# Kernel tuning notes

Hardware: AMD Instinct MI355X
Metric: run time of the kernel (lower is better)

The kernel has to match this reference:

```python
import jax, jax.numpy as jnp
import numpy as np

TOK_DIM = 512
POS_DIM = 512
N_HEADS = 16
HEAD_DIM = 64
D_MODEL = 1024
INNER = N_HEADS * HEAD_DIM
B, T = 4, 2048


def setup_inputs() -> dict:
    key = jax.random.key(0)
    ks = jax.random.split(key, 5)
    s = 0.02
    return {
        "x": jax.random.normal(ks[0], (B, T, TOK_DIM + POS_DIM), dtype=jnp.float32),
        "Wq": jax.random.normal(ks[1], (POS_DIM, INNER), dtype=jnp.float32) * s,
        "Wk": jax.random.normal(ks[2], (POS_DIM, INNER), dtype=jnp.float32) * s,
        "Wv": jax.random.normal(ks[3], (TOK_DIM, INNER), dtype=jnp.float32) * s,
        "Wo": jax.random.normal(ks[4], (INNER, D_MODEL), dtype=jnp.float32) * s,
    }


def reference(x, Wq, Wk, Wv, Wo):
    b, t, _ = x.shape
    x_tok = x[:, :, :TOK_DIM]
    x_pos = x[:, :, TOK_DIM:]
    # project and split heads: [B, H, T, Dh]
    q = (x_pos @ Wq).reshape(b, t, N_HEADS, HEAD_DIM).transpose(0, 2, 1, 3)
    k = (x_pos @ Wk).reshape(b, t, N_HEADS, HEAD_DIM).transpose(0, 2, 1, 3)
    v = (x_tok @ Wv).reshape(b, t, N_HEADS, HEAD_DIM).transpose(0, 2, 1, 3)
    att = jnp.einsum("bhqd,bhkd->bhqk", q, k) / jnp.sqrt(jnp.float32(HEAD_DIM))
    causal = jnp.tril(jnp.ones((t, t), dtype=bool))
    att = jnp.where(causal, att, -jnp.inf)
    att = jax.nn.softmax(att, axis=-1)
    out = jnp.einsum("bhqk,bhkd->bhqd", att, v)
    out = out.transpose(0, 2, 1, 3).reshape(b, t, INNER)
    return out @ Wo
```

## Files before the change

### kernel.cpp

```cpp
#include <hip/hip_runtime.h>
#include <stdint.h>


typedef unsigned short u16;
typedef __bf16 bf16;
typedef bf16 bf16x8 __attribute__((ext_vector_type(8)));
typedef u16 u16x8 __attribute__((ext_vector_type(8)));
typedef u16 u16x4 __attribute__((ext_vector_type(4)));
typedef float f32x4 __attribute__((ext_vector_type(4)));
typedef uint32_t u32x4 __attribute__((ext_vector_type(4)));

__device__ __forceinline__ u16 cvt_bf16(float f) {
  uint32_t u = __builtin_bit_cast(uint32_t, f);
  u += 0x7FFFu + ((u >> 16) & 1u);
  return (u16)(u >> 16);
}

__device__ __forceinline__ uint32_t pack2_bf16(float lo, float hi) {
  uint32_t a = __builtin_bit_cast(uint32_t, lo) + 0x8000u;
  uint32_t b = __builtin_bit_cast(uint32_t, hi) + 0x8000u;
  return __builtin_amdgcn_perm(b, a, 0x07060302u);
}

__device__ __forceinline__ f32x4 mfma_bf(bf16x8 a, bf16x8 b, f32x4 c) {
  return __builtin_amdgcn_mfma_f32_16x16x32_bf16(a, b, c, 0, 0, 0);
}

typedef __attribute__((address_space(1))) const uint32_t g_u32;
typedef __attribute__((address_space(3))) uint32_t l_u32;
__device__ __forceinline__ void gload16(const u16* g, u16* l) {
  __builtin_amdgcn_global_load_lds((g_u32*)g, (l_u32*)l, 16, 0, 0);
}

__global__ __launch_bounds__(256) void prep_x(
    const float* __restrict__ x, u16* __restrict__ xtok,
    u16* __restrict__ xpos) {
  int idx = blockIdx.x * 256 + threadIdx.x;
  int row = idx >> 8;
  int c4 = (idx & 255) * 4;
  float4 v = *(const float4*)(x + (size_t)row * 1024 + c4);
  u16x4 b = {cvt_bf16(v.x), cvt_bf16(v.y), cvt_bf16(v.z), cvt_bf16(v.w)};
  u16* dst = (c4 < 512) ? (xtok + (size_t)row * 512 + c4)
                        : (xpos + (size_t)row * 512 + c4 - 512);
  *(u16x4*)dst = b;
}

__global__ __launch_bounds__(256) void prep_w(
    const float* __restrict__ Wq, const float* __restrict__ Wk,
    const float* __restrict__ Wv, const float* __restrict__ Wo,
    u16* __restrict__ Wt, u16* __restrict__ WoT) {
  const int z = blockIdx.z;
  const float* src = (z == 0) ? Wq : (z == 1) ? Wk : (z == 2) ? Wv : Wo;
  const int K = (z == 3) ? 1024 : 512;
  u16* dst = (z == 3) ? WoT : (Wt + (size_t)z * 1024 * 512);
  const int k0 = blockIdx.y * 64, n0 = blockIdx.x * 64;
  if (k0 >= K) return;
  __shared__ u16 T[64][68];
  const int tid = threadIdx.x;
  const int r = tid >> 4, c = (tid & 15) * 4;
#pragma unroll
  for (int i = 0; i < 4; i++) {
    float4 v = *(const float4*)(src + (size_t)(k0 + r + i * 16) * 1024 + n0 + c);
    u16x4 b = {cvt_bf16(v.x), cvt_bf16(v.y), cvt_bf16(v.z), cvt_bf16(v.w)};
    *(u16x4*)&T[r + i * 16][c] = b;
  }
  __syncthreads();
#pragma unroll
  for (int i = 0; i < 4; i++) {
    int n = r + i * 16;
    u16x4 v;
#pragma unroll
    for (int j = 0; j < 4; j++) v[j] = T[c + j][n];
    *(u16x4*)(dst + (size_t)(n0 + n) * K + k0 + c) = v;
  }
}


#define LDA(P, S) { const u16* bp_ = rA + (P)*16384 + (S)*8192;              \
  af[0][0] = *(const bf16x8*)(bp_ + 0*1024 + colx0);                         \
  af[0][1] = *(const bf16x8*)(bp_ + 0*1024 + colx1);                         \
  af[1][0] = *(const bf16x8*)(bp_ + 1*1024 + colx0);                         \
  af[1][1] = *(const bf16x8*)(bp_ + 1*1024 + colx1);                         \
  af[2][0] = *(const bf16x8*)(bp_ + 2*1024 + colx0);                         \
  af[2][1] = *(const bf16x8*)(bp_ + 2*1024 + colx1);                         \
  af[3][0] = *(const bf16x8*)(bp_ + 3*1024 + colx0);                         \
  af[3][1] = *(const bf16x8*)(bp_ + 3*1024 + colx1); }

#define LDB(P, S, NB) { const u16* bp_ = rB + (P)*16384 + (S)*8192;          \
  bf[(NB)+0][0] = *(const bf16x8*)(bp_ + 0*1024 + colx0);                    \
  bf[(NB)+0][1] = *(const bf16x8*)(bp_ + 0*1024 + colx1);                    \
  bf[(NB)+1][0] = *(const bf16x8*)(bp_ + 1*1024 + colx0);                    \
  bf[(NB)+1][1] = *(const bf16x8*)(bp_ + 1*1024 + colx1); }

#define MM1(M_, N_, J_) { f32x4 c_ = acc[M_][N_];                            \
  c_ = mfma_bf(af[J_][0], bf[N_][0], c_);                                    \
  c_ = mfma_bf(af[J_][1], bf[N_][1], c_);                                    \
  acc[M_][N_] = c_; }

#define MM(MB, NB) MM1((MB)+0,(NB)+0,0) MM1((MB)+0,(NB)+1,0)                 \
                   MM1((MB)+1,(NB)+0,1) MM1((MB)+1,(NB)+1,1)                 \
                   MM1((MB)+2,(NB)+0,2) MM1((MB)+2,(NB)+1,2)                 \
                   MM1((MB)+3,(NB)+0,3) MM1((MB)+3,(NB)+1,3)

#define STA(P, S, KT) { const u16* s_ = gA + (size_t)(S)*64*Kd + (KT)*64;    \
  u16* d_ = lA + (P)*16384 + (S)*8192;                                       \
  gload16(s_, d_); gload16(s_ + (size_t)128*Kd, d_ + 4096); }

#define STB(P, S, KT) { const u16* s_ = gB + (size_t)(S)*32*Kd + (KT)*64;    \
  u16* d_ = lB + (P)*16384 + (S)*8192;                                       \
  gload16(s_, d_); gload16(s_ + (size_t)128*Kd, d_ + 4096); }

#define PH_MID  asm volatile("" ::: "memory"); __builtin_amdgcn_s_barrier(); \
  asm volatile("s_waitcnt lgkmcnt(0)" ::: "memory");                         \
  __builtin_amdgcn_s_setprio(1);

#define PH_END  __builtin_amdgcn_s_setprio(0);                               \
  asm volatile("" ::: "memory"); __builtin_amdgcn_s_barrier();

#define PH_END_VM  __builtin_amdgcn_s_setprio(0);                            \
  asm volatile("s_waitcnt vmcnt(6)" ::: "memory");                           \
  asm volatile("" ::: "memory"); __builtin_amdgcn_s_barrier();

template <int Kd>
__device__ __forceinline__ void gemm256_core(
    const u16* __restrict__ Aptr, const u16* __restrict__ Bptr,
    int m0, int n0, u16* smem, f32x4 (&acc)[8][4]) {
  constexpr int NKT = Kd / 64;
  constexpr int NI = NKT / 2;
  const int tid = threadIdx.x;
  const int lane = tid & 63;
  const int mrow = lane & 15, quad = lane >> 4;
  const int w = tid >> 6, wm2 = w >> 2, wn4 = w & 3;

  u16* As = smem;
  u16* Bs = smem + 32768;

  const int lrs = tid >> 3, sp8 = tid & 7;
  const int slog = sp8 ^ (lrs & 7);
  const u16* gA = Aptr + (size_t)(m0 + (lrs & 63)) * Kd + slog * 8;
  const u16* gB =
      Bptr + (size_t)(n0 + ((lrs >> 5) << 6) + (lrs & 31)) * Kd + slog * 8;
  u16* lA = As + tid * 8;
  u16* lB = Bs + tid * 8;

  const int colx0 = (quad * 8) ^ ((mrow & 7) * 8);
  const int colx1 = (32 + quad * 8) ^ ((mrow & 7) * 8);
  const u16* rA = As + (wm2 * 64 + mrow) * 64;
  const u16* rB = Bs + (wn4 * 32 + mrow) * 64;

  bf16x8 af[4][2], bf[4][2];

  STA(0, 0, 0) STB(0, 0, 0) STB(0, 1, 0) STA(0, 1, 0)
  STA(1, 0, 1) STB(1, 0, 1) STB(1, 1, 1)
  asm volatile("s_waitcnt vmcnt(6)" ::: "memory");
  asm volatile("" ::: "memory");
  __builtin_amdgcn_s_barrier();

  for (int i = 0; i < NI; ++i) {
    const int kt1 = 2 * i + 1;
    const int kt2 = (2 * i + 2 < NKT) ? 2 * i + 2 : NKT - 1;
    const int kt3 = (2 * i + 3 < NKT) ? 2 * i + 3 : NKT - 1;
    LDA(0, 0) LDB(0, 0, 0) STA(1, 1, kt1)
    PH_MID MM(0, 0) PH_END
    LDB(0, 1, 2) STA(0, 0, kt2)
    PH_MID MM(0, 2) PH_END
    LDA(0, 1) STB(0, 0, kt2)
    PH_MID MM(4, 2) PH_END
    STB(0, 1, kt2)
    PH_MID MM(4, 0) PH_END_VM
    LDA(1, 0) LDB(1, 0, 0) STA(0, 1, kt2)
    PH_MID MM(0, 0) PH_END
    LDB(1, 1, 2) STA(1, 0, kt3)
    PH_MID MM(0, 2) PH_END
    LDA(1, 1) STB(1, 0, kt3)
    PH_MID MM(4, 2) PH_END
    STB(1, 1, kt3)
    PH_MID MM(4, 0) PH_END_VM
  }
  asm volatile("s_waitcnt vmcnt(0)" ::: "memory");
  __builtin_amdgcn_s_barrier();
}

__global__ __launch_bounds__(512, 2) void gemm_qkv256(
    const u16* __restrict__ xtok, const u16* __restrict__ xpos,
    const u16* __restrict__ Wt, u16* __restrict__ qkv,
    u16* __restrict__ vperm) {
  const int z = blockIdx.z;
  const u16* A = (z == 2) ? xtok : xpos;
  const u16* Bt = Wt + (size_t)z * 1024 * 512;
  u16* outp = qkv + (size_t)z * (64u * 2048u * 64u);
  const float osc = (z == 0) ? 0.18033688011112042f : 1.0f;
  const int m0 = blockIdx.y * 256, n0 = blockIdx.x * 256;

  __shared__ __align__(16) u16 smem[65536];
  f32x4 acc[8][4];
#pragma unroll
  for (int i = 0; i < 8; i++)
#pragma unroll
    for (int j = 0; j < 4; j++) acc[i][j] = (f32x4){0.f, 0.f, 0.f, 0.f};

  gemm256_core<512>(A, Bt, m0, n0, smem, acc);

  const int tid = threadIdx.x;
  const int lane = tid & 63;
  const int mrow = lane & 15, quad = lane >> 4;
  const int w = tid >> 6, wm2 = w >> 2, wn4 = w & 3;

  if (z != 2) {
#pragma unroll
    for (int mi = 0; mi < 8; mi++)
#pragma unroll
      for (int ni = 0; ni < 4; ni++)
#pragma unroll
        for (int r = 0; r < 4; r++) {
          int m = m0 + wm2 * 128 + mi * 16 + quad * 4 + r;
          int n = n0 + wn4 * 64 + ni * 16 + mrow;
          int bb = m >> 11, t = m & 2047;
          int h = n >> 6, d = n & 63;
          outp[(((size_t)(bb * 16 + h)) * 2048 + t) * 64 + d] =
              cvt_bf16(acc[mi][ni][r] * osc);
        }
  } else {
#pragma unroll
    for (int mi = 0; mi < 8; mi++)
#pragma unroll
      for (int ni = 0; ni < 4; ni++)
#pragma unroll
        for (int r = 0; r < 4; r++) {
          int m = m0 + wm2 * 128 + mi * 16 + quad * 4 + r;
          int n = n0 + wn4 * 64 + ni * 16 + mrow;
          int bb = m >> 11, t = m & 2047;
          int h = n >> 6, d = n & 63;
          int k6 = t & 63;
          int pos = (k6 & 32) + ((k6 >> 4) & 1) * 4 + ((k6 >> 2) & 3) * 8 +
                    (k6 & 3);
          vperm[(((size_t)(bb * 16 + h)) * 64 + d) * 2048 + (t & ~63) + pos] =
              cvt_bf16(acc[mi][ni][r]);
        }
  }
}

__global__ __launch_bounds__(512, 2) void gemm_out256(
    const u16* __restrict__ Am, const u16* __restrict__ WoT,
    float* __restrict__ out) {
  const int m0 = blockIdx.y * 256, n0 = blockIdx.x * 256;

  __shared__ __align__(16) u16 smem[65536];
  f32x4 acc[8][4];
#pragma unroll
  for (int i = 0; i < 8; i++)
#pragma unroll
    for (int j = 0; j < 4; j++) acc[i][j] = (f32x4){0.f, 0.f, 0.f, 0.f};

  gemm256_core<1024>(Am, WoT, m0, n0, smem, acc);

  const int tid = threadIdx.x;
  const int lane = tid & 63;
  const int mrow = lane & 15, quad = lane >> 4;
  const int w = tid >> 6, wm2 = w >> 2, wn4 = w & 3;

#pragma unroll
  for (int mi = 0; mi < 8; mi++)
#pragma unroll
    for (int ni = 0; ni < 4; ni++)
#pragma unroll
      for (int r = 0; r < 4; r++) {
        int m = m0 + wm2 * 128 + mi * 16 + quad * 4 + r;
        int n = n0 + wn4 * 64 + ni * 16 + mrow;
        out[(size_t)m * 1024 + n] = acc[mi][ni][r];
      }
}

__global__ __launch_bounds__(256, 2) void attn(
    const u16* __restrict__ qkv, const u16* __restrict__ vperm,
    u16* __restrict__ aout) {
  const int bh = blockIdx.x;
  const int sp = blockIdx.y;
  const int bb = bh >> 4, h = bh & 15;
  const u16* Qp = qkv + (size_t)bh * (2048 * 64);
  const u16* Kp = qkv + (size_t)(64 + bh) * (2048 * 64);
  const u16* Vp = vperm + (size_t)bh * (64 * 2048);

  __shared__ __align__(16) u16 Ksh0[64 * 32], Ksh1[64 * 32];
  __shared__ __align__(16) u16 Vsh0[64 * 32], Vsh1[64 * 32];
  __shared__ __align__(16) u16 Osh[4][32][72];

  const int tid = threadIdx.x;
  const int lane = tid & 63;
  const int w = tid >> 6;
  const int mrow = lane & 15;
  const int quad = lane >> 4;
  const int srow = w * 16 + (lane >> 2);
  const int sc = (lane & 3) * 8;

  const u16x8 onesu = {0x3F80, 0x3F80, 0x3F80, 0x3F80,
                       0x3F80, 0x3F80, 0x3F80, 0x3F80};
  const bf16x8 ones = __builtin_bit_cast(bf16x8, onesu);

  const u16* kgb = Kp + (size_t)srow * 64 + sc;
  const u16* vgb = Vp + (size_t)srow * 2048 + sc;

  for (int half = 0; half < 2; ++half) {
    const int qt = (half == 0) ? sp : 15 - sp;
    const int q0 = qt * 128;
    const int nk = 2 * qt + 2;
    const int qw = q0 + w * 32;

    const u16* qbase = Qp + (size_t)(qw + mrow) * 64 + quad * 8;
    const bf16x8 qf00 = *(const bf16x8*)qbase;
    const bf16x8 qf01 = *(const bf16x8*)(qbase + 32);
    const bf16x8 qf10 = *(const bf16x8*)(qbase + 16 * 64);
    const bf16x8 qf11 = *(const bf16x8*)(qbase + 16 * 64 + 32);

    f32x4 o[2][4], ol[2];
#pragma unroll
    for (int g = 0; g < 2; ++g) {
#pragma unroll
      for (int dt = 0; dt < 4; ++dt) o[g][dt] = (f32x4){0.f, 0.f, 0.f, 0.f};
      ol[g] = (f32x4){0.f, 0.f, 0.f, 0.f};
    }

    u16x8 ka0 = *(const u16x8*)kgb;
    u16x8 ka1 = *(const u16x8*)(kgb + 32);
    u16x8 va0 = *(const u16x8*)vgb;
    u16x8 va1 = *(const u16x8*)(vgb + 32);

    for (int it = 0; it < nk; ++it) {
      __syncthreads();
      *(u16x8*)(Ksh0 + srow * 32 + sc) = ka0;
      *(u16x8*)(Ksh1 + srow * 32 + sc) = ka1;
      *(u16x8*)(Vsh0 + srow * 32 + sc) = va0;
      *(u16x8*)(Vsh1 + srow * 32 + sc) = va1;
      __syncthreads();

      if (it + 1 < nk) {
        const int kn = (it + 1) * 64;
        ka0 = *(const u16x8*)(kgb + (size_t)kn * 64);
        ka1 = *(const u16x8*)(kgb + (size_t)kn * 64 + 32);
        va0 = *(const u16x8*)(vgb + kn);
        va1 = *(const u16x8*)(vgb + kn + 32);
      }

      const int k0 = it * 64;
      if (k0 > qw + 31) continue;

      f32x4 s[2][4];
#pragma unroll
      for (int nt = 0; nt < 4; ++nt) {
        bf16x8 kf0 = *(const bf16x8*)(Ksh0 + (nt * 16 + mrow) * 32 + quad * 8);
        bf16x8 kf1 = *(const bf16x8*)(Ksh1 + (nt * 16 + mrow) * 32 + quad * 8);
        f32x4 z0 = (f32x4){0.f, 0.f, 0.f, 0.f};
        z0 = mfma_bf(kf0, qf00, z0);
        s[0][nt] = mfma_bf(kf1, qf01, z0);
        f32x4 z1 = (f32x4){0.f, 0.f, 0.f, 0.f};
        z1 = mfma_bf(kf0, qf10, z1);
        s[1][nt] = mfma_bf(kf1, qf11, z1);
      }

      if (k0 + 63 > qw) {
#pragma unroll
        for (int g = 0; g < 2; ++g)
#pragma unroll
          for (int nt = 0; nt < 4; ++nt)
#pragma unroll
            for (int r = 0; r < 4; ++r)
              if (k0 + nt * 16 + quad * 4 + r > qw + g * 16 + mrow)
                s[g][nt][r] = -1e30f;
      }
#pragma unroll
      for (int g = 0; g < 2; ++g)
#pragma unroll
        for (int nt = 0; nt < 4; ++nt)
#pragma unroll
          for (int r = 0; r < 4; ++r)
            s[g][nt][r] = __builtin_amdgcn_exp2f(s[g][nt][r]);

      bf16x8 pf[2][2];
#pragma unroll
      for (int g = 0; g < 2; ++g) {
        u32x4 pw0 = {pack2_bf16(s[g][0][0], s[g][0][1]),
                     pack2_bf16(s[g][0][2], s[g][0][3]),
                     pack2_bf16(s[g][1][0], s[g][1][1]),
                     pack2_bf16(s[g][1][2], s[g][1][3])};
        u32x4 pw1 = {pack2_bf16(s[g][2][0], s[g][2][1]),
                     pack2_bf16(s[g][2][2], s[g][2][3]),
                     pack2_bf16(s[g][3][0], s[g][3][1]),
                     pack2_bf16(s[g][3][2], s[g][3][3])};
        pf[g][0] = __builtin_bit_cast(bf16x8, pw0);
        pf[g][1] = __builtin_bit_cast(bf16x8, pw1);
        ol[g] = mfma_bf(ones, pf[g][0], ol[g]);
        ol[g] = mfma_bf(ones, pf[g][1], ol[g]);
      }

#pragma unroll
      for (int dt = 0; dt < 4; ++dt) {
        bf16x8 vf0 = *(const bf16x8*)(Vsh0 + (dt * 16 + mrow) * 32 + quad * 8);
        bf16x8 vf1 = *(const bf16x8*)(Vsh1 + (dt * 16 + mrow) * 32 + quad * 8);
        o[0][dt] = mfma_bf(vf0, pf[0][0], o[0][dt]);
        o[0][dt] = mfma_bf(vf1, pf[0][1], o[0][dt]);
        o[1][dt] = mfma_bf(vf0, pf[1][0], o[1][dt]);
        o[1][dt] = mfma_bf(vf1, pf[1][1], o[1][dt]);
      }
    }

#pragma unroll
    for (int g = 0; g < 2; ++g) {
      const float inv = 1.f / ol[g][0];
#pragma unroll
      for (int dt = 0; dt < 4; ++dt)
#pragma unroll
        for (int r = 0; r < 4; ++r)
          Osh[w][g * 16 + mrow][dt * 16 + quad * 4 + r] =
              cvt_bf16(o[g][dt][r] * inv);
    }
#pragma unroll
    for (int p = 0; p < 4; ++p) {
      int ql = (lane >> 3) + 8 * p;
      int ch = lane & 7;
      u16x8 v = *(const u16x8*)&Osh[w][ql][ch * 8];
      int t = q0 + w * 32 + ql;
      *(u16x8*)(aout + ((size_t)(bb * 2048 + t)) * 1024 + h * 64 + ch * 8) = v;
    }
  }
}

extern "C" void kernel_launch(void* const* d_in, const int* in_sizes, int n_in,
                              void* d_out, int out_size, void* d_ws, size_t ws_size,
                              hipStream_t stream) {
  const float* x  = (const float*)d_in[0];
  const float* Wq = (const float*)d_in[1];
  const float* Wk = (const float*)d_in[2];
  const float* Wv = (const float*)d_in[3];
  const float* Wo = (const float*)d_in[4];

  u16* qkv   = (u16*)d_ws;
  u16* vperm = qkv + (size_t)3 * 64 * 2048 * 64;
  u16* aout  = vperm + (size_t)64 * 64 * 2048;
  u16* xtok  = aout + (size_t)8192 * 1024;
  u16* xpos  = xtok + (size_t)8192 * 512;
  u16* Wt    = xpos + (size_t)8192 * 512;
  u16* WoT   = Wt + (size_t)3 * 1024 * 512;
  float* out = (float*)d_out;

  prep_x<<<dim3(8192), dim3(256), 0, stream>>>(x, xtok, xpos);
  prep_w<<<dim3(16, 16, 4), dim3(256), 0, stream>>>(Wq, Wk, Wv, Wo, Wt, WoT);
  gemm_qkv256<<<dim3(4, 32, 3), dim3(512), 0, stream>>>(xtok, xpos, Wt, qkv, vperm);
  attn<<<dim3(64, 8), dim3(256), 0, stream>>>(qkv, vperm, aout);
  gemm_out256<<<dim3(4, 32), dim3(512), 0, stream>>>(aout, WoT, out);
}
```

Baseline: 206.9 us.

## Split attention into one q-tile per block, longest-first, with hardware bf16 pack

The attention kernel no longer pairs two causal q-tiles (sp and 15-sp) inside one block. It launches 16 blocks per head, ordered from the longest tile to the shortest, and raises the launch-bounds occupancy hint from 2 to 4. The manual round-and-permute bf16 packing is replaced with the v_cvt_pk_bf16_f32 instruction, and s_setprio is raised around the MFMA sections. The aim is more resident waves and better load balance, at the cost of tighter register limits (possible spills) and duplicated per-block setup.

```diff
diff --git a/kernel.cpp b/kernel.cpp
--- a/kernel.cpp
+++ b/kernel.cpp
@@ -16,10 +16,10 @@
   return (u16)(u >> 16);
 }
 
-__device__ __forceinline__ uint32_t pack2_bf16(float lo, float hi) {
-  uint32_t a = __builtin_bit_cast(uint32_t, lo) + 0x8000u;
-  uint32_t b = __builtin_bit_cast(uint32_t, hi) + 0x8000u;
-  return __builtin_amdgcn_perm(b, a, 0x07060302u);
+__device__ __forceinline__ uint32_t cvtpk_bf16(float lo, float hi) {
+  uint32_t r;
+  asm("v_cvt_pk_bf16_f32 %0, %1, %2" : "=v"(r) : "v"(lo), "v"(hi));
+  return r;
 }
 
 __device__ __forceinline__ f32x4 mfma_bf(bf16x8 a, bf16x8 b, f32x4 c) {
@@ -271,11 +271,11 @@
       }
 }
 
-__global__ __launch_bounds__(256, 2) void attn(
+__global__ __launch_bounds__(256, 4) void attn(
     const u16* __restrict__ qkv, const u16* __restrict__ vperm,
     u16* __restrict__ aout) {
   const int bh = blockIdx.x;
-  const int sp = blockIdx.y;
+  const int qt = 15 - blockIdx.y;
   const int bb = bh >> 4, h = bh & 15;
   const u16* Qp = qkv + (size_t)bh * (2048 * 64);
   const u16* Kp = qkv + (size_t)(64 + bh) * (2048 * 64);
@@ -300,127 +300,130 @@
   const u16* kgb = Kp + (size_t)srow * 64 + sc;
   const u16* vgb = Vp + (size_t)srow * 2048 + sc;
 
-  for (int half = 0; half < 2; ++half) {
-    const int qt = (half == 0) ? sp : 15 - sp;
-    const int q0 = qt * 128;
-    const int nk = 2 * qt + 2;
-    const int qw = q0 + w * 32;
-
-    const u16* qbase = Qp + (size_t)(qw + mrow) * 64 + quad * 8;
-    const bf16x8 qf00 = *(const bf16x8*)qbase;
-    const bf16x8 qf01 = *(const bf16x8*)(qbase + 32);
-    const bf16x8 qf10 = *(const bf16x8*)(qbase + 16 * 64);
-    const bf16x8 qf11 = *(const bf16x8*)(qbase + 16 * 64 + 32);
-
-    f32x4 o[2][4], ol[2];
+  const int q0 = qt * 128;
+  const int nk = 2 * qt + 2;
+  const int qw = q0 + w * 32;
+
+  const u16* qbase = Qp + (size_t)(qw + mrow) * 64 + quad * 8;
+  const bf16x8 qf00 = *(const bf16x8*)qbase;
+  const bf16x8 qf01 = *(const bf16x8*)(qbase + 32);
+  const bf16x8 qf10 = *(const bf16x8*)(qbase + 16 * 64);
+  const bf16x8 qf11 = *(const bf16x8*)(qbase + 16 * 64 + 32);
+
+  f32x4 o[2][4], ol[2];
+#pragma unroll
+  for (int g = 0; g < 2; ++g) {
+#pragma unroll
+    for (int dt = 0; dt < 4; ++dt) o[g][dt] = (f32x4){0.f, 0.f, 0.f, 0.f};
+    ol[g] = (f32x4){0.f, 0.f, 0.f, 0.f};
+  }
+
+  u16x8 ka0 = *(const u16x8*)kgb;
+  u16x8 ka1 = *(const u16x8*)(kgb + 32);
+  u16x8 va0 = *(const u16x8*)vgb;
+  u16x8 va1 = *(const u16x8*)(vgb + 32);
+
+  for (int it = 0; it < nk; ++it) {
+    __syncthreads();
+    *(u16x8*)(Ksh0 + srow * 32 + sc) = ka0;
+    *(u16x8*)(Ksh1 + srow * 32 + sc) = ka1;
+    *(u16x8*)(Vsh0 + srow * 32 + sc) = va0;
+    *(u16x8*)(Vsh1 + srow * 32 + sc) = va1;
+    __syncthreads();
+
+    if (it + 1 < nk) {
+      const int kn = (it + 1) * 64;
+      ka0 = *(const u16x8*)(kgb + (size_t)kn * 64);
+      ka1 = *(const u16x8*)(kgb + (size_t)kn * 64 + 32);
+      va0 = *(const u16x8*)(vgb + kn);
+      va1 = *(const u16x8*)(vgb + kn + 32);
+    }
+
+    const int k0 = it * 64;
+    if (k0 > qw + 31) continue;
+
+    f32x4 s[2][4];
+    __builtin_amdgcn_s_setprio(1);
+#pragma unroll
+    for (int nt = 0; nt < 4; ++nt) {
+      bf16x8 kf0 = *(const bf16x8*)(Ksh0 + (nt * 16 + mrow) * 32 + quad * 8);
+      bf16x8 kf1 = *(const bf16x8*)(Ksh1 + (nt * 16 + mrow) * 32 + quad * 8);
+      f32x4 z0 = (f32x4){0.f, 0.f, 0.f, 0.f};
+      z0 = mfma_bf(kf0, qf00, z0);
+      s[0][nt] = mfma_bf(kf1, qf01, z0);
+      f32x4 z1 = (f32x4){0.f, 0.f, 0.f, 0.f};
+      z1 = mfma_bf(kf0, qf10, z1);
+      s[1][nt] = mfma_bf(kf1, qf11, z1);
+    }
+    __builtin_amdgcn_s_setprio(0);
+
+    if (k0 + 63 > qw) {
+#pragma unroll
+      for (int g = 0; g < 2; ++g)
+#pragma unroll
+        for (int nt = 0; nt < 4; ++nt)
+#pragma unroll
+          for (int r = 0; r < 4; ++r)
+            if (k0 + nt * 16 + quad * 4 + r > qw + g * 16 + mrow)
+              s[g][nt][r] = -1e30f;
+    }
+#pragma unroll
+    for (int g = 0; g < 2; ++g)
+#pragma unroll
+      for (int nt = 0; nt < 4; ++nt)
+#pragma unroll
+        for (int r = 0; r < 4; ++r)
+          s[g][nt][r] = __builtin_amdgcn_exp2f(s[g][nt][r]);
+
+    bf16x8 pf[2][2];
 #pragma unroll
     for (int g = 0; g < 2; ++g) {
-#pragma unroll
-      for (int dt = 0; dt < 4; ++dt) o[g][dt] = (f32x4){0.f, 0.f, 0.f, 0.f};
-      ol[g] = (f32x4){0.f, 0.f, 0.f, 0.f};
+      u32x4 pw0 = {cvtpk_bf16(s[g][0][0], s[g][0][1]),
+                   cvtpk_bf16(s[g][0][2], s[g][0][3]),
+                   cvtpk_bf16(s[g][1][0], s[g][1][1]),
+                   cvtpk_bf16(s[g][1][2], s[g][1][3])};
+      u32x4 pw1 = {cvtpk_bf16(s[g][2][0], s[g][2][1]),
+                   cvtpk_bf16(s[g][2][2], s[g][2][3]),
+                   cvtpk_bf16(s[g][3][0], s[g][3][1]),
+                   cvtpk_bf16(s[g][3][2], s[g][3][3])};
+      pf[g][0] = __builtin_bit_cast(bf16x8, pw0);
+      pf[g][1] = __builtin_bit_cast(bf16x8, pw1);
     }
 
-    u16x8 ka0 = *(const u16x8*)kgb;
-    u16x8 ka1 = *(const u16x8*)(kgb + 32);
-    u16x8 va0 = *(const u16x8*)vgb;
-    u16x8 va1 = *(const u16x8*)(vgb + 32);
-
-    for (int it = 0; it < nk; ++it) {
-      __syncthreads();
-      *(u16x8*)(Ksh0 + srow * 32 + sc) = ka0;
-      *(u16x8*)(Ksh1 + srow * 32 + sc) = ka1;
-      *(u16x8*)(Vsh0 + srow * 32 + sc) = va0;
-      *(u16x8*)(Vsh1 + srow * 32 + sc) = va1;
-      __syncthreads();
-
-      if (it + 1 < nk) {
-        const int kn = (it + 1) * 64;
-        ka0 = *(const u16x8*)(kgb + (size_t)kn * 64);
-        ka1 = *(const u16x8*)(kgb + (size_t)kn * 64 + 32);
-        va0 = *(const u16x8*)(vgb + kn);
-        va1 = *(const u16x8*)(vgb + kn + 32);
-      }
-
-      const int k0 = it * 64;
-      if (k0 > qw + 31) continue;
-
-      f32x4 s[2][4];
-#pragma unroll
-      for (int nt = 0; nt < 4; ++nt) {
-        bf16x8 kf0 = *(const bf16x8*)(Ksh0 + (nt * 16 + mrow) * 32 + quad * 8);
-        bf16x8 kf1 = *(const bf16x8*)(Ksh1 + (nt * 16 + mrow) * 32 + quad * 8);
-        f32x4 z0 = (f32x4){0.f, 0.f, 0.f, 0.f};
-        z0 = mfma_bf(kf0, qf00, z0);
-        s[0][nt] = mfma_bf(kf1, qf01, z0);
-        f32x4 z1 = (f32x4){0.f, 0.f, 0.f, 0.f};
-        z1 = mfma_bf(kf0, qf10, z1);
-        s[1][nt] = mfma_bf(kf1, qf11, z1);
-      }
-
-      if (k0 + 63 > qw) {
-#pragma unroll
-        for (int g = 0; g < 2; ++g)
-#pragma unroll
-          for (int nt = 0; nt < 4; ++nt)
-#pragma unroll
-            for (int r = 0; r < 4; ++r)
-              if (k0 + nt * 16 + quad * 4 + r > qw + g * 16 + mrow)
-                s[g][nt][r] = -1e30f;
-      }
-#pragma unroll
-      for (int g = 0; g < 2; ++g)
-#pragma unroll
-        for (int nt = 0; nt < 4; ++nt)
-#pragma unroll
-          for (int r = 0; r < 4; ++r)
-            s[g][nt][r] = __builtin_amdgcn_exp2f(s[g][nt][r]);
-
-      bf16x8 pf[2][2];
-#pragma unroll
-      for (int g = 0; g < 2; ++g) {
-        u32x4 pw0 = {pack2_bf16(s[g][0][0], s[g][0][1]),
-                     pack2_bf16(s[g][0][2], s[g][0][3]),
-                     pack2_bf16(s[g][1][0], s[g][1][1]),
-                     pack2_bf16(s[g][1][2], s[g][1][3])};
-        u32x4 pw1 = {pack2_bf16(s[g][2][0], s[g][2][1]),
-                     pack2_bf16(s[g][2][2], s[g][2][3]),
-                     pack2_bf16(s[g][3][0], s[g][3][1]),
-                     pack2_bf16(s[g][3][2], s[g][3][3])};
-        pf[g][0] = __builtin_bit_cast(bf16x8, pw0);
-        pf[g][1] = __builtin_bit_cast(bf16x8, pw1);
-        ol[g] = mfma_bf(ones, pf[g][0], ol[g]);
-        ol[g] = mfma_bf(ones, pf[g][1], ol[g]);
-      }
-
-#pragma unroll
-      for (int dt = 0; dt < 4; ++dt) {
-        bf16x8 vf0 = *(const bf16x8*)(Vsh0 + (dt * 16 + mrow) * 32 + quad * 8);
-        bf16x8 vf1 = *(const bf16x8*)(Vsh1 + (dt * 16 + mrow) * 32 + quad * 8);
-        o[0][dt] = mfma_bf(vf0, pf[0][0], o[0][dt]);
-        o[0][dt] = mfma_bf(vf1, pf[0][1], o[0][dt]);
-        o[1][dt] = mfma_bf(vf0, pf[1][0], o[1][dt]);
-        o[1][dt] = mfma_bf(vf1, pf[1][1], o[1][dt]);
-      }
+    __builtin_amdgcn_s_setprio(1);
+    ol[0] = mfma_bf(ones, pf[0][0], ol[0]);
+    ol[0] = mfma_bf(ones, pf[0][1], ol[0]);
+    ol[1] = mfma_bf(ones, pf[1][0], ol[1]);
+    ol[1] = mfma_bf(ones, pf[1][1], ol[1]);
+#pragma unroll
+    for (int dt = 0; dt < 4; ++dt) {
+      bf16x8 vf0 = *(const bf16x8*)(Vsh0 + (dt * 16 + mrow) * 32 + quad * 8);
+      bf16x8 vf1 = *(const bf16x8*)(Vsh1 + (dt * 16 + mrow) * 32 + quad * 8);
+      o[0][dt] = mfma_bf(vf0, pf[0][0], o[0][dt]);
+      o[0][dt] = mfma_bf(vf1, pf[0][1], o[0][dt]);
+      o[1][dt] = mfma_bf(vf0, pf[1][0], o[1][dt]);
+      o[1][dt] = mfma_bf(vf1, pf[1][1], o[1][dt]);
     }
-
-#pragma unroll
-    for (int g = 0; g < 2; ++g) {
-      const float inv = 1.f / ol[g][0];
-#pragma unroll
-      for (int dt = 0; dt < 4; ++dt)
-#pragma unroll
-        for (int r = 0; r < 4; ++r)
-          Osh[w][g * 16 + mrow][dt * 16 + quad * 4 + r] =
-              cvt_bf16(o[g][dt][r] * inv);
-    }
-#pragma unroll
-    for (int p = 0; p < 4; ++p) {
-      int ql = (lane >> 3) + 8 * p;
-      int ch = lane & 7;
-      u16x8 v = *(const u16x8*)&Osh[w][ql][ch * 8];
-      int t = q0 + w * 32 + ql;
-      *(u16x8*)(aout + ((size_t)(bb * 2048 + t)) * 1024 + h * 64 + ch * 8) = v;
-    }
+    __builtin_amdgcn_s_setprio(0);
+  }
+
+#pragma unroll
+  for (int g = 0; g < 2; ++g) {
+    const float inv = 1.f / ol[g][0];
+#pragma unroll
+    for (int dt = 0; dt < 4; ++dt)
+#pragma unroll
+      for (int r = 0; r < 4; ++r)
+        Osh[w][g * 16 + mrow][dt * 16 + quad * 4 + r] =
+            cvt_bf16(o[g][dt][r] * inv);
+  }
+#pragma unroll
+  for (int p = 0; p < 4; ++p) {
+    int ql = (lane >> 3) + 8 * p;
+    int ch = lane & 7;
+    u16x8 v = *(const u16x8*)&Osh[w][ql][ch * 8];
+    int t = q0 + w * 32 + ql;
+    *(u16x8*)(aout + ((size_t)(bb * 2048 + t)) * 1024 + h * 64 + ch * 8) = v;
   }
 }
 
@@ -445,6 +448,6 @@
   prep_x<<<dim3(8192), dim3(256), 0, stream>>>(x, xtok, xpos);
   prep_w<<<dim3(16, 16, 4), dim3(256), 0, stream>>>(Wq, Wk, Wv, Wo, Wt, WoT);
   gemm_qkv256<<<dim3(4, 32, 3), dim3(512), 0, stream>>>(xtok, xpos, Wt, qkv, vperm);
-  attn<<<dim3(64, 8), dim3(256), 0, stream>>>(qkv, vperm, aout);
+  attn<<<dim3(64, 16), dim3(256), 0, stream>>>(qkv, vperm, aout);
   gemm_out256<<<dim3(4, 32), dim3(512), 0, stream>>>(aout, WoT, out);
 }
```

New measurement: 218.7 us. 1.06x slower.

## Double-buffer attention K/V tiles, drop paired q-tiles, launch one block per tile

Applied to the files above, without the earlier changes.

The attention kernel now gives each q-tile its own block (grid 64x16, heaviest tiles first) instead of pairing tile sp with 15-sp inside one block. K/V staging in shared memory becomes double-buffered, so only one barrier per iteration is needed instead of two. The output staging buffer reuses the K/V shared memory, and launch bounds are raised to 4 blocks per CU. This aims for more occupancy and less barrier stall, at the cost of losing the built-in load balancing from pairing tiles and leaving scheduling to the hardware.

```diff
diff --git a/kernel.cpp b/kernel.cpp
--- a/kernel.cpp
+++ b/kernel.cpp
@@ -271,19 +271,17 @@
       }
 }
 
-__global__ __launch_bounds__(256, 2) void attn(
+__global__ __launch_bounds__(256, 4) void attn(
     const u16* __restrict__ qkv, const u16* __restrict__ vperm,
     u16* __restrict__ aout) {
   const int bh = blockIdx.x;
-  const int sp = blockIdx.y;
+  const int qt = 15 - blockIdx.y;
   const int bb = bh >> 4, h = bh & 15;
   const u16* Qp = qkv + (size_t)bh * (2048 * 64);
   const u16* Kp = qkv + (size_t)(64 + bh) * (2048 * 64);
   const u16* Vp = vperm + (size_t)bh * (64 * 2048);
 
-  __shared__ __align__(16) u16 Ksh0[64 * 32], Ksh1[64 * 32];
-  __shared__ __align__(16) u16 Vsh0[64 * 32], Vsh1[64 * 32];
-  __shared__ __align__(16) u16 Osh[4][32][72];
+  __shared__ __align__(16) u16 smem[2][4][64 * 32];
 
   const int tid = threadIdx.x;
   const int lane = tid & 63;
@@ -292,6 +290,7 @@
   const int quad = lane >> 4;
   const int srow = w * 16 + (lane >> 2);
   const int sc = (lane & 3) * 8;
+  const int soff = srow * 32 + sc;
 
   const u16x8 onesu = {0x3F80, 0x3F80, 0x3F80, 0x3F80,
                        0x3F80, 0x3F80, 0x3F80, 0x3F80};
@@ -300,127 +299,128 @@
   const u16* kgb = Kp + (size_t)srow * 64 + sc;
   const u16* vgb = Vp + (size_t)srow * 2048 + sc;
 
-  for (int half = 0; half < 2; ++half) {
-    const int qt = (half == 0) ? sp : 15 - sp;
-    const int q0 = qt * 128;
-    const int nk = 2 * qt + 2;
-    const int qw = q0 + w * 32;
-
-    const u16* qbase = Qp + (size_t)(qw + mrow) * 64 + quad * 8;
-    const bf16x8 qf00 = *(const bf16x8*)qbase;
-    const bf16x8 qf01 = *(const bf16x8*)(qbase + 32);
-    const bf16x8 qf10 = *(const bf16x8*)(qbase + 16 * 64);
-    const bf16x8 qf11 = *(const bf16x8*)(qbase + 16 * 64 + 32);
-
-    f32x4 o[2][4], ol[2];
+  const int q0 = qt * 128;
+  const int nk = 2 * qt + 2;
+  const int qw = q0 + w * 32;
+
+  const u16* qbase = Qp + (size_t)(qw + mrow) * 64 + quad * 8;
+  const bf16x8 qf00 = *(const bf16x8*)qbase;
+  const bf16x8 qf01 = *(const bf16x8*)(qbase + 32);
+  const bf16x8 qf10 = *(const bf16x8*)(qbase + 16 * 64);
+  const bf16x8 qf11 = *(const bf16x8*)(qbase + 16 * 64 + 32);
+
+  f32x4 o[2][4], ol[2];
+#pragma unroll
+  for (int g = 0; g < 2; ++g) {
+#pragma unroll
+    for (int dt = 0; dt < 4; ++dt) o[g][dt] = (f32x4){0.f, 0.f, 0.f, 0.f};
+    ol[g] = (f32x4){0.f, 0.f, 0.f, 0.f};
+  }
+
+  u16x8 ka0 = *(const u16x8*)kgb;
+  u16x8 ka1 = *(const u16x8*)(kgb + 32);
+  u16x8 va0 = *(const u16x8*)vgb;
+  u16x8 va1 = *(const u16x8*)(vgb + 32);
+
+  for (int it = 0; it < nk; ++it) {
+    u16* buf = &smem[it & 1][0][0];
+    *(u16x8*)(buf + 0 * 2048 + soff) = ka0;
+    *(u16x8*)(buf + 1 * 2048 + soff) = ka1;
+    *(u16x8*)(buf + 2 * 2048 + soff) = va0;
+    *(u16x8*)(buf + 3 * 2048 + soff) = va1;
+
+    if (it + 1 < nk) {
+      const int kn = (it + 1) * 64;
+      ka0 = *(const u16x8*)(kgb + (size_t)kn * 64);
+      ka1 = *(const u16x8*)(kgb + (size_t)kn * 64 + 32);
+      va0 = *(const u16x8*)(vgb + kn);
+      va1 = *(const u16x8*)(vgb + kn + 32);
+    }
+
+    __syncthreads();
+
+    const int k0 = it * 64;
+    if (k0 > qw + 31) continue;
+
+    f32x4 s[2][4];
+#pragma unroll
+    for (int nt = 0; nt < 4; ++nt) {
+      bf16x8 kf0 = *(const bf16x8*)(buf + 0 * 2048 + (nt * 16 + mrow) * 32 + quad * 8);
+      bf16x8 kf1 = *(const bf16x8*)(buf + 1 * 2048 + (nt * 16 + mrow) * 32 + quad * 8);
+      f32x4 z0 = (f32x4){0.f, 0.f, 0.f, 0.f};
+      z0 = mfma_bf(kf0, qf00, z0);
+      s[0][nt] = mfma_bf(kf1, qf01, z0);
+      f32x4 z1 = (f32x4){0.f, 0.f, 0.f, 0.f};
+      z1 = mfma_bf(kf0, qf10, z1);
+      s[1][nt] = mfma_bf(kf1, qf11, z1);
+    }
+
+    if (k0 + 63 > qw) {
+#pragma unroll
+      for (int g = 0; g < 2; ++g)
+#pragma unroll
+        for (int nt = 0; nt < 4; ++nt)
+#pragma unroll
+          for (int r = 0; r < 4; ++r)
+            if (k0 + nt * 16 + quad * 4 + r > qw + g * 16 + mrow)
+              s[g][nt][r] = -1e30f;
+    }
+#pragma unroll
+    for (int g = 0; g < 2; ++g)
+#pragma unroll
+      for (int nt = 0; nt < 4; ++nt)
+#pragma unroll
+        for (int r = 0; r < 4; ++r)
+          s[g][nt][r] = __builtin_amdgcn_exp2f(s[g][nt][r]);
+
+    bf16x8 pf[2][2];
 #pragma unroll
     for (int g = 0; g < 2; ++g) {
-#pragma unroll
-      for (int dt = 0; dt < 4; ++dt) o[g][dt] = (f32x4){0.f, 0.f, 0.f, 0.f};
-      ol[g] = (f32x4){0.f, 0.f, 0.f, 0.f};
+      u32x4 pw0 = {pack2_bf16(s[g][0][0], s[g][0][1]),
+                   pack2_bf16(s[g][0][2], s[g][0][3]),
+                   pack2_bf16(s[g][1][0], s[g][1][1]),
+                   pack2_bf16(s[g][1][2], s[g][1][3])};
+      u32x4 pw1 = {pack2_bf16(s[g][2][0], s[g][2][1]),
+                   pack2_bf16(s[g][2][2], s[g][2][3]),
+                   pack2_bf16(s[g][3][0], s[g][3][1]),
+                   pack2_bf16(s[g][3][2], s[g][3][3])};
+      pf[g][0] = __builtin_bit_cast(bf16x8, pw0);
+      pf[g][1] = __builtin_bit_cast(bf16x8, pw1);
+      ol[g] = mfma_bf(ones, pf[g][0], ol[g]);
+      ol[g] = mfma_bf(ones, pf[g][1], ol[g]);
     }
 
-    u16x8 ka0 = *(const u16x8*)kgb;
-    u16x8 ka1 = *(const u16x8*)(kgb + 32);
-    u16x8 va0 = *(const u16x8*)vgb;
-    u16x8 va1 = *(const u16x8*)(vgb + 32);
-
-    for (int it = 0; it < nk; ++it) {
-      __syncthreads();
-      *(u16x8*)(Ksh0 + srow * 32 + sc) = ka0;
-      *(u16x8*)(Ksh1 + srow * 32 + sc) = ka1;
-      *(u16x8*)(Vsh0 + srow * 32 + sc) = va0;
-      *(u16x8*)(Vsh1 + srow * 32 + sc) = va1;
-      __syncthreads();
-
-      if (it + 1 < nk) {
-        const int kn = (it + 1) * 64;
-        ka0 = *(const u16x8*)(kgb + (size_t)kn * 64);
-        ka1 = *(const u16x8*)(kgb + (size_t)kn * 64 + 32);
-        va0 = *(const u16x8*)(vgb + kn);
-        va1 = *(const u16x8*)(vgb + kn + 32);
-      }
-
-      const int k0 = it * 64;
-      if (k0 > qw + 31) continue;
-
-      f32x4 s[2][4];
-#pragma unroll
-      for (int nt = 0; nt < 4; ++nt) {
-        bf16x8 kf0 = *(const bf16x8*)(Ksh0 + (nt * 16 + mrow) * 32 + quad * 8);
-        bf16x8 kf1 = *(const bf16x8*)(Ksh1 + (nt * 16 + mrow) * 32 + quad * 8);
-        f32x4 z0 = (f32x4){0.f, 0.f, 0.f, 0.f};
-        z0 = mfma_bf(kf0, qf00, z0);
-        s[0][nt] = mfma_bf(kf1, qf01, z0);
-        f32x4 z1 = (f32x4){0.f, 0.f, 0.f, 0.f};
-        z1 = mfma_bf(kf0, qf10, z1);
-        s[1][nt] = mfma_bf(kf1, qf11, z1);
-      }
-
-      if (k0 + 63 > qw) {
-#pragma unroll
-        for (int g = 0; g < 2; ++g)
-#pragma unroll
-          for (int nt = 0; nt < 4; ++nt)
-#pragma unroll
-            for (int r = 0; r < 4; ++r)
-              if (k0 + nt * 16 + quad * 4 + r > qw + g * 16 + mrow)
-                s[g][nt][r] = -1e30f;
-      }
-#pragma unroll
-      for (int g = 0; g < 2; ++g)
-#pragma unroll
-        for (int nt = 0; nt < 4; ++nt)
-#pragma unroll
-          for (int r = 0; r < 4; ++r)
-            s[g][nt][r] = __builtin_amdgcn_exp2f(s[g][nt][r]);
-
-      bf16x8 pf[2][2];
-#pragma unroll
-      for (int g = 0; g < 2; ++g) {
-        u32x4 pw0 = {pack2_bf16(s[g][0][0], s[g][0][1]),
-                     pack2_bf16(s[g][0][2], s[g][0][3]),
-                     pack2_bf16(s[g][1][0], s[g][1][1]),
-                     pack2_bf16(s[g][1][2], s[g][1][3])};
-        u32x4 pw1 = {pack2_bf16(s[g][2][0], s[g][2][1]),
-                     pack2_bf16(s[g][2][2], s[g][2][3]),
-                     pack2_bf16(s[g][3][0], s[g][3][1]),
-                     pack2_bf16(s[g][3][2], s[g][3][3])};
-        pf[g][0] = __builtin_bit_cast(bf16x8, pw0);
-        pf[g][1] = __builtin_bit_cast(bf16x8, pw1);
-        ol[g] = mfma_bf(ones, pf[g][0], ol[g]);
-        ol[g] = mfma_bf(ones, pf[g][1], ol[g]);
-      }
-
-#pragma unroll
-      for (int dt = 0; dt < 4; ++dt) {
-        bf16x8 vf0 = *(const bf16x8*)(Vsh0 + (dt * 16 + mrow) * 32 + quad * 8);
-        bf16x8 vf1 = *(const bf16x8*)(Vsh1 + (dt * 16 + mrow) * 32 + quad * 8);
-        o[0][dt] = mfma_bf(vf0, pf[0][0], o[0][dt]);
-        o[0][dt] = mfma_bf(vf1, pf[0][1], o[0][dt]);
-        o[1][dt] = mfma_bf(vf0, pf[1][0], o[1][dt]);
-        o[1][dt] = mfma_bf(vf1, pf[1][1], o[1][dt]);
-      }
+#pragma unroll
+    for (int dt = 0; dt < 4; ++dt) {
+      bf16x8 vf0 = *(const bf16x8*)(buf + 2 * 2048 + (dt * 16 + mrow) * 32 + quad * 8);
+      bf16x8 vf1 = *(const bf16x8*)(buf + 3 * 2048 + (dt * 16 + mrow) * 32 + quad * 8);
+      o[0][dt] = mfma_bf(vf0, pf[0][0], o[0][dt]);
+      o[0][dt] = mfma_bf(vf1, pf[0][1], o[0][dt]);
+      o[1][dt] = mfma_bf(vf0, pf[1][0], o[1][dt]);
+      o[1][dt] = mfma_bf(vf1, pf[1][1], o[1][dt]);
     }
-
-#pragma unroll
-    for (int g = 0; g < 2; ++g) {
-      const float inv = 1.f / ol[g][0];
-#pragma unroll
-      for (int dt = 0; dt < 4; ++dt)
-#pragma unroll
-        for (int r = 0; r < 4; ++r)
-          Osh[w][g * 16 + mrow][dt * 16 + quad * 4 + r] =
-              cvt_bf16(o[g][dt][r] * inv);
-    }
-#pragma unroll
-    for (int p = 0; p < 4; ++p) {
-      int ql = (lane >> 3) + 8 * p;
-      int ch = lane & 7;
-      u16x8 v = *(const u16x8*)&Osh[w][ql][ch * 8];
-      int t = q0 + w * 32 + ql;
-      *(u16x8*)(aout + ((size_t)(bb * 2048 + t)) * 1024 + h * 64 + ch * 8) = v;
-    }
+  }
+
+  __syncthreads();
+  u16* Osh = &smem[0][0][0];
+
+#pragma unroll
+  for (int g = 0; g < 2; ++g) {
+    const float inv = 1.f / ol[g][0];
+#pragma unroll
+    for (int dt = 0; dt < 4; ++dt)
+#pragma unroll
+      for (int r = 0; r < 4; ++r)
+        Osh[(w * 32 + g * 16 + mrow) * 72 + dt * 16 + quad * 4 + r] =
+            cvt_bf16(o[g][dt][r] * inv);
+  }
+#pragma unroll
+  for (int p = 0; p < 4; ++p) {
+    int ql = (lane >> 3) + 8 * p;
+    int ch = lane & 7;
+    u16x8 v = *(const u16x8*)&Osh[(w * 32 + ql) * 72 + ch * 8];
+    int t = q0 + w * 32 + ql;
+    *(u16x8*)(aout + ((size_t)(bb * 2048 + t)) * 1024 + h * 64 + ch * 8) = v;
   }
 }
 
@@ -445,6 +445,6 @@
   prep_x<<<dim3(8192), dim3(256), 0, stream>>>(x, xtok, xpos);
   prep_w<<<dim3(16, 16, 4), dim3(256), 0, stream>>>(Wq, Wk, Wv, Wo, Wt, WoT);
   gemm_qkv256<<<dim3(4, 32, 3), dim3(512), 0, stream>>>(xtok, xpos, Wt, qkv, vperm);
-  attn<<<dim3(64, 8), dim3(256), 0, stream>>>(qkv, vperm, aout);
+  attn<<<dim3(64, 16), dim3(256), 0, stream>>>(qkv, vperm, aout);
   gemm_out256<<<dim3(4, 32), dim3(512), 0, stream>>>(aout, WoT, out);
 }
```

Measured after the change: 208.2 us. No clear change (+0.6%).
